# Kernel optimization log

Measured on AMD Instinct MI355X. Metric: run time of the kernel, lower is better.

## Reference

```python
import jax, jax.numpy as jnp
import numpy as np

DIM = 192
SHIFT = 3
PAD = SHIFT // 2  # 1
EPS = 1e-5


def conv1x1(x, w, b):
    # 1x1x1 Conv3d == channel matmul. x: (B,C,D,H,W), w: (O,C), b: (O,)
    return jnp.einsum('bcdhw,oc->bodhw', x, w) + b[None, :, None, None, None]


def group_norm1(x, w, b):
    # GroupNorm(1, C): normalize over (C,D,H,W) per sample, per-channel affine.
    mu = x.mean(axis=(1, 2, 3, 4), keepdims=True)
    var = x.var(axis=(1, 2, 3, 4), keepdims=True)
    xn = (x - mu) * jax.lax.rsqrt(var + EPS)
    return xn * w[None, :, None, None, None] + b[None, :, None, None, None]


def axial_shift(x, axis):
    # reflect-pad all 3 spatial dims, roll channel-chunks along `axis`, crop back.
    R = x.shape[-1]
    xp = jnp.pad(x, ((0, 0), (0, 0), (PAD, PAD), (PAD, PAD), (PAD, PAD)), mode='reflect')
    chunks = jnp.split(xp, SHIFT, axis=1)
    rolled = [jnp.roll(c, s, axis=axis) for c, s in zip(chunks, range(-PAD, PAD + 1))]
    xc = jnp.concatenate(rolled, axis=1)
    return xc[:, :, PAD:PAD + R, PAD:PAD + R, PAD:PAD + R]


def setup_inputs() -> dict:
    key = jax.random.key(0)
    ks = jax.random.split(key, 16)
    B, C, R = 8, DIM, 32
    x = jax.random.normal(ks[0], (B, C, R, R, R), dtype=jnp.float32)
    wmat = lambda k: jax.random.normal(k, (C, C), dtype=jnp.float32) * 0.05
    vec = lambda k: jax.random.normal(k, (C,), dtype=jnp.float32) * 0.05
    return {
        'x': x,
        'w1': wmat(ks[1]), 'b1': vec(ks[2]),
        'n1w': jnp.ones((C,), jnp.float32), 'n1b': jnp.zeros((C,), jnp.float32),
        'w21': wmat(ks[3]), 'b21': vec(ks[4]),
        'w22': wmat(ks[5]), 'b22': vec(ks[6]),
        'w23': wmat(ks[7]), 'b23': vec(ks[8]),
        'n2w': jnp.ones((C,), jnp.float32), 'n2b': jnp.zeros((C,), jnp.float32),
        'w3': wmat(ks[9]), 'b3': vec(ks[10]),
    }


def reference(x, w1, b1, n1w, n1b, w21, b21, w22, b22, w23, b23, n2w, n2b, w3, b3):
    h = conv1x1(x, w1, b1)
    h = group_norm1(h, n1w, n1b)
    h = jax.nn.gelu(h, approximate=False)
    h = axial_shift(h, axis=3)
    h = conv1x1(h, w22, b22)
    h = axial_shift(h, axis=2)
    h = conv1x1(h, w21, b21)
    h = axial_shift(h, axis=4)
    h = conv1x1(h, w23, b23)
    h = jax.nn.gelu(h, approximate=False)
    h = group_norm1(h, n2w, n2b)
    h = conv1x1(h, w3, b3)
    return h
```

## Files before the change

kernel.cpp:

```cpp
#include <hip/hip_runtime.h>
#include <math.h>

#define NCH 192
#define NB 8
#define SPAT 32768
#define TILES_PER_B 512
#define NBLK (NB * TILES_PER_B)
#define NELEM_PER_B ((size_t)NCH * SPAT)

typedef short s16x8 __attribute__((ext_vector_type(8)));
typedef float f32x4 __attribute__((ext_vector_type(4)));

__device__ __forceinline__ float bf2f(unsigned short h) {
  return __uint_as_float(((unsigned)h) << 16);
}
__device__ __forceinline__ unsigned short f2bf(float f) {
  unsigned u = __float_as_uint(f);
  u += 0x7FFF + ((u >> 16) & 1);
  return (unsigned short)(u >> 16);
}
__device__ __forceinline__ unsigned cvt_pk(float lo, float hi) {
  unsigned r;
  asm("v_cvt_pk_bf16_f32 %0, %1, %2" : "=v"(r) : "v"(lo), "v"(hi));
  return r;
}

__device__ __forceinline__ float gelu_f(float x) {
  float x2 = x * x;
  float z2 = x * fmaf(x2, 0.0713548163f, 1.5957769100f);
  float e = __expf(z2);
  float r = __builtin_amdgcn_rcpf(e + 1.0f);
  return fmaf(-r, x, x);
}

__device__ __forceinline__ int rshift(int i, int c) {
  int j = i - (c - 1);
  j = (j < 0) ? 1 : j;
  j = (j > 31) ? 30 : j;
  return j;
}

__device__ __forceinline__ int lds_off(int c, int p, int u) {
  return (c * 64 + p) * 128 + 16 * (((u >> 3) ^ (p & 7) ^ ((p >> 3) & 7)) & 7) + 2 * (u & 7);
}

template <int SHIFTW>
__device__ __forceinline__ void do_gemm48(const char* __restrict__ B,
                                          const unsigned short* __restrict__ wm,
                                          int wave, int col, int kg,
                                          f32x4 acc[3][4]) {
  const unsigned short* wp = wm + (wave * 48 + col) * NCH + kg * 8;
  s16x8 afc[3], afn[3];
#pragma unroll
  for (int r = 0; r < 3; ++r) afc[r] = *(const s16x8*)(wp + r * 16 * NCH);
#pragma unroll
  for (int ks = 0; ks < 6; ++ks) {
    if (ks < 5) {
#pragma unroll
      for (int r = 0; r < 3; ++r)
        afn[r] = *(const s16x8*)(wp + (ks + 1) * 32 + r * 16 * NCH);
    }
    int k0 = ks * 32 + kg * 8;
    int c = k0 >> 6, u = k0 & 63;
    s16x8 bf[4];
#pragma unroll
    for (int m = 0; m < 4; ++m) {
      int p = m * 16 + col;
      int ps = SHIFTW ? ((p & 32) | rshift(p & 31, c)) : p;
      bf[m] = *(const s16x8*)(B + lds_off(c, ps, u));
    }
#pragma unroll
    for (int r = 0; r < 3; ++r)
#pragma unroll
      for (int m = 0; m < 4; ++m)
        acc[r][m] = __builtin_amdgcn_mfma_f32_16x16x32_bf16(afc[r], bf[m], acc[r][m], 0, 0, 0);
#pragma unroll
    for (int r = 0; r < 3; ++r) afc[r] = afn[r];
  }
}

__device__ __forceinline__ void stats_reduce(float ssum, float ssq, int wave, int lane,
                                             float* red, float* partials, int blk) {
#pragma unroll
  for (int off = 1; off < 64; off <<= 1) {
    ssum += __shfl_xor(ssum, off, 64);
    ssq += __shfl_xor(ssq, off, 64);
  }
  if (lane == 0) { red[wave * 2] = ssum; red[wave * 2 + 1] = ssq; }
  __syncthreads();
  if (wave == 0 && lane == 0) {
    partials[blk * 2] = red[0] + red[2] + red[4] + red[6];
    partials[blk * 2 + 1] = red[1] + red[3] + red[5] + red[7];
  }
}

__device__ __forceinline__ void store_tile(const char* __restrict__ L, char* __restrict__ ob,
                                           int tid) {
  int G = tid & 7;
#pragma unroll
  for (int j = 0; j < 6; ++j) {
    const int c = j >> 1;
    int p = (j & 1) * 32 + (tid >> 3);
    s16x8 v = *(const s16x8*)(L + lds_off(c, p, G * 8));
    *(s16x8*)(ob + (size_t)p * 384 + (c * 8 + G) * 16) = v;
  }
}

__global__ __launch_bounds__(256, 4)
void pass1(const float* __restrict__ x, const unsigned short* __restrict__ w1b,
           const float* __restrict__ b1, unsigned short* __restrict__ out,
           float* __restrict__ partials) {
  __shared__ __align__(16) char B[3 * 64 * 128];
  __shared__ float red[8];
  int blk = blockIdx.x, b = blk >> 9, p0 = (blk & 511) * 64;
  int tid = threadIdx.x, wave = tid >> 6, lane = tid & 63;
  int col = lane & 15, kg = lane >> 4;

  const float* xb = x + (size_t)b * NELEM_PER_B + p0;
  int q = tid & 15;
#pragma unroll
  for (int j = 0; j < 6; ++j) {
    int chp = j * 16 + (tid >> 4);
    int ch0 = 2 * chp;
    int cc = chp >> 5, u0 = ch0 & 63;
    const float* s0 = xb + (size_t)ch0 * SPAT + 4 * q;
    f32x4 a = *(const f32x4*)s0;
    f32x4 c2 = *(const f32x4*)(s0 + SPAT);
#pragma unroll
    for (int i = 0; i < 4; ++i)
      *(unsigned*)(B + lds_off(cc, 4 * q + i, u0)) = cvt_pk(a[i], c2[i]);
  }
  __syncthreads();

  f32x4 acc[3][4] = {};
  do_gemm48<0>(B, w1b, wave, col, kg, acc);

  float ssum = 0.f, ssq = 0.f;
  __syncthreads();
#pragma unroll
  for (int r = 0; r < 3; ++r) {
    int rowb = wave * 48 + r * 16 + kg * 4;
    f32x4 bs = *(const f32x4*)(b1 + rowb);
#pragma unroll
    for (int m = 0; m < 4; ++m) {
      int p = m * 16 + col;
      float v0 = acc[r][m][0] + bs[0], v1 = acc[r][m][1] + bs[1];
      float v2 = acc[r][m][2] + bs[2], v3 = acc[r][m][3] + bs[3];
      ssum += (v0 + v1) + (v2 + v3);
      ssq = fmaf(v0, v0, fmaf(v1, v1, fmaf(v2, v2, fmaf(v3, v3, ssq))));
      uint2 pk; pk.x = cvt_pk(v0, v1); pk.y = cvt_pk(v2, v3);
      *(uint2*)(B + lds_off(rowb >> 6, p, rowb & 63)) = pk;
    }
  }
  __syncthreads();
  store_tile(B, (char*)out + ((size_t)b * SPAT + p0) * 384, tid);
  stats_reduce(ssum, ssq, wave, lane, red, partials, blk);
}

__global__ __launch_bounds__(256, 4)
void pass2a(const unsigned short* __restrict__ in, const unsigned short* __restrict__ w22b,
            const float* __restrict__ b22, unsigned short* __restrict__ out,
            const unsigned short* __restrict__ ACbf) {
  __shared__ __align__(16) char B[3 * 64 * 128];
  int blk = blockIdx.x, b = blk >> 9, p0 = (blk & 511) * 64;
  int tid = threadIdx.x, wave = tid >> 6, lane = tid & 63;
  int col = lane & 15, kg = lane >> 4;

  const char* ib = (const char*)in + (size_t)b * SPAT * 384;
  const unsigned short* acb = ACbf + b * 2 * NCH;
  int G = tid & 7;
#pragma unroll
  for (int j = 0; j < 6; ++j) {
    const int c = j >> 1;
    int p = (j & 1) * 32 + (tid >> 3);
    int h = ((p0 + p) >> 5) & 31;
    int sp = (p0 + p) + (rshift(h, c) - h) * 32;
    s16x8 v = *(const s16x8*)(ib + (size_t)sp * 384 + (c * 8 + G) * 16);
    s16x8 aA = *(const s16x8*)(acb + c * 64 + G * 8);
    s16x8 aC = *(const s16x8*)(acb + NCH + c * 64 + G * 8);
    unsigned w[4];
#pragma unroll
    for (int i = 0; i < 4; ++i) {
      float f0 = gelu_f(fmaf(bf2f((unsigned short)v[2 * i]), bf2f((unsigned short)aA[2 * i]),
                             bf2f((unsigned short)aC[2 * i])));
      float f1 = gelu_f(fmaf(bf2f((unsigned short)v[2 * i + 1]), bf2f((unsigned short)aA[2 * i + 1]),
                             bf2f((unsigned short)aC[2 * i + 1])));
      w[i] = cvt_pk(f0, f1);
    }
    *(uint2*)(B + lds_off(c, p, G * 8)) = make_uint2(w[0], w[1]);
    *(uint2*)(B + lds_off(c, p, G * 8 + 4)) = make_uint2(w[2], w[3]);
  }
  __syncthreads();

  f32x4 acc[3][4] = {};
  do_gemm48<0>(B, w22b, wave, col, kg, acc);
  __syncthreads();
#pragma unroll
  for (int r = 0; r < 3; ++r) {
    int rowb = wave * 48 + r * 16 + kg * 4;
    f32x4 bs = *(const f32x4*)(b22 + rowb);
#pragma unroll
    for (int m = 0; m < 4; ++m) {
      int p = m * 16 + col;
      uint2 pk;
      pk.x = cvt_pk(acc[r][m][0] + bs[0], acc[r][m][1] + bs[1]);
      pk.y = cvt_pk(acc[r][m][2] + bs[2], acc[r][m][3] + bs[3]);
      *(uint2*)(B + lds_off(rowb >> 6, p, rowb & 63)) = pk;
    }
  }
  __syncthreads();
  store_tile(B, (char*)out + ((size_t)b * SPAT + p0) * 384, tid);
}

__global__ __launch_bounds__(256, 4)
void pass2bc(const unsigned short* __restrict__ in, const unsigned short* __restrict__ w21b,
             const float* __restrict__ b21, const unsigned short* __restrict__ w23b,
             const float* __restrict__ b23, unsigned short* __restrict__ out,
             float* __restrict__ partials) {
  __shared__ __align__(16) char B[3 * 64 * 128];
  __shared__ float red[8];
  int blk = blockIdx.x, b = blk >> 9, p0 = (blk & 511) * 64;
  int tid = threadIdx.x, wave = tid >> 6, lane = tid & 63;
  int col = lane & 15, kg = lane >> 4;

  int d = p0 >> 10;
  int soff[3];
#pragma unroll
  for (int c = 0; c < 3; ++c) soff[c] = (rshift(d, c) - d) * 1024;

  const char* ib = (const char*)in + (size_t)b * SPAT * 384;
  int G = tid & 7;
#pragma unroll
  for (int j = 0; j < 6; ++j) {
    const int c = j >> 1;
    int p = (j & 1) * 32 + (tid >> 3);
    s16x8 v = *(const s16x8*)(ib + (size_t)(p0 + p + soff[c]) * 384 + (c * 8 + G) * 16);
    *(s16x8*)(B + lds_off(c, p, G * 8)) = v;
  }
  __syncthreads();

  f32x4 acc[3][4] = {};
  do_gemm48<0>(B, w21b, wave, col, kg, acc);
  __syncthreads();
#pragma unroll
  for (int r = 0; r < 3; ++r) {
    int rowb = wave * 48 + r * 16 + kg * 4;
    f32x4 bs = *(const f32x4*)(b21 + rowb);
#pragma unroll
    for (int m = 0; m < 4; ++m) {
      int p = m * 16 + col;
      uint2 pk;
      pk.x = cvt_pk(acc[r][m][0] + bs[0], acc[r][m][1] + bs[1]);
      pk.y = cvt_pk(acc[r][m][2] + bs[2], acc[r][m][3] + bs[3]);
      *(uint2*)(B + lds_off(rowb >> 6, p, rowb & 63)) = pk;
    }
  }
  __syncthreads();

#pragma unroll
  for (int r = 0; r < 3; ++r)
#pragma unroll
    for (int m = 0; m < 4; ++m) acc[r][m] = (f32x4){0.f, 0.f, 0.f, 0.f};
  do_gemm48<1>(B, w23b, wave, col, kg, acc);
  __syncthreads();

  float ssum = 0.f, ssq = 0.f;
#pragma unroll
  for (int r = 0; r < 3; ++r) {
    int rowb = wave * 48 + r * 16 + kg * 4;
    f32x4 bs = *(const f32x4*)(b23 + rowb);
#pragma unroll
    for (int m = 0; m < 4; ++m) {
      int p = m * 16 + col;
      float v0 = gelu_f(acc[r][m][0] + bs[0]), v1 = gelu_f(acc[r][m][1] + bs[1]);
      float v2 = gelu_f(acc[r][m][2] + bs[2]), v3 = gelu_f(acc[r][m][3] + bs[3]);
      ssum += (v0 + v1) + (v2 + v3);
      ssq = fmaf(v0, v0, fmaf(v1, v1, fmaf(v2, v2, fmaf(v3, v3, ssq))));
      uint2 pk; pk.x = cvt_pk(v0, v1); pk.y = cvt_pk(v2, v3);
      *(uint2*)(B + lds_off(rowb >> 6, p, rowb & 63)) = pk;
    }
  }
  __syncthreads();
  store_tile(B, (char*)out + ((size_t)b * SPAT + p0) * 384, tid);
  stats_reduce(ssum, ssq, wave, lane, red, partials, blk);
}

__global__ __launch_bounds__(256, 4)
void pass3(const unsigned short* __restrict__ in, const unsigned short* __restrict__ w3e,
           const float* __restrict__ b3e, float* __restrict__ outf) {
  __shared__ __align__(16) char B[3 * 64 * 128];
  int blk = blockIdx.x, b = blk >> 9, p0 = (blk & 511) * 64;
  int tid = threadIdx.x, wave = tid >> 6, lane = tid & 63;
  int col = lane & 15, kg = lane >> 4;

  const char* ib = (const char*)in + (size_t)b * SPAT * 384;
  int G = tid & 7;
#pragma unroll
  for (int j = 0; j < 6; ++j) {
    const int c = j >> 1;
    int p = (j & 1) * 32 + (tid >> 3);
    s16x8 v = *(const s16x8*)(ib + (size_t)(p0 + p) * 384 + (c * 8 + G) * 16);
    *(s16x8*)(B + lds_off(c, p, G * 8)) = v;
  }
  __syncthreads();

  f32x4 acc[3][4] = {};
  do_gemm48<0>(B, w3e + (size_t)b * NCH * NCH, wave, col, kg, acc);

  const float* bb = b3e + b * NCH;
#pragma unroll
  for (int r = 0; r < 3; ++r) {
    int rowb = wave * 48 + r * 16 + kg * 4;
    f32x4 bs = *(const f32x4*)(bb + rowb);
#pragma unroll
    for (int m = 0; m < 4; ++m) {
      int p = p0 + m * 16 + col;
#pragma unroll
      for (int j = 0; j < 4; ++j)
        outf[((size_t)b * NCH + rowb + j) * SPAT + p] = acc[r][m][j] + bs[j];
    }
  }
}

__global__ void stats_finalize(const float* __restrict__ partials,
                               const float* __restrict__ nw, const float* __restrict__ nb,
                               float* __restrict__ AC, unsigned short* __restrict__ ACbf) {
  int b = blockIdx.x, tid = threadIdx.x;
  __shared__ float s0[256], s1[256];
  float a = 0.f, c = 0.f;
  for (int i = tid; i < TILES_PER_B; i += 256) {
    a += partials[(b * TILES_PER_B + i) * 2];
    c += partials[(b * TILES_PER_B + i) * 2 + 1];
  }
  s0[tid] = a; s1[tid] = c;
  __syncthreads();
  for (int st = 128; st > 0; st >>= 1) {
    if (tid < st) { s0[tid] += s0[tid + st]; s1[tid] += s1[tid + st]; }
    __syncthreads();
  }
  float inv_n = 1.0f / (float)NELEM_PER_B;
  float mu = s0[0] * inv_n;
  float var = s1[0] * inv_n - mu * mu;
  float rs = rsqrtf(var + 1e-5f);
  if (tid < NCH) {
    float A = rs * nw[tid];
    float C = nb[tid] - mu * A;
    AC[b * 2 * NCH + tid] = A;
    AC[b * 2 * NCH + NCH + tid] = C;
    ACbf[b * 2 * NCH + tid] = f2bf(A);
    ACbf[b * 2 * NCH + NCH + tid] = f2bf(C);
  }
}

__global__ void prep_weights(const float* __restrict__ w1, const float* __restrict__ w21,
                             const float* __restrict__ w22, const float* __restrict__ w23,
                             unsigned short* __restrict__ wb) {
  int i = blockIdx.x * 256 + threadIdx.x;
  if (i >= 4 * NCH * NCH) return;
  int m = i / (NCH * NCH), r = i % (NCH * NCH);
  const float* src = (m == 0) ? w1 : (m == 1) ? w22 : (m == 2) ? w21 : w23;
  wb[i] = f2bf(src[r]);
}

__global__ void prep_w3(const float* __restrict__ w3, const float* __restrict__ b3,
                        const float* __restrict__ AC2,
                        unsigned short* __restrict__ w3e, float* __restrict__ b3e) {
  int b = blockIdx.x, o = threadIdx.x;
  if (o >= NCH) return;
  const float* A = AC2 + b * 2 * NCH;
  const float* C = A + NCH;
  float s = b3[o];
  for (int c = 0; c < NCH; ++c) {
    float w = w3[o * NCH + c];
    w3e[((size_t)b * NCH + o) * NCH + c] = f2bf(w * A[c]);
    s = fmaf(w, C[c], s);
  }
  b3e[b * NCH + o] = s;
}

extern "C" void kernel_launch(void* const* d_in, const int* in_sizes, int n_in,
                              void* d_out, int out_size, void* d_ws, size_t ws_size,
                              hipStream_t stream) {
  const float* x   = (const float*)d_in[0];
  const float* w1  = (const float*)d_in[1];
  const float* b1  = (const float*)d_in[2];
  const float* n1w = (const float*)d_in[3];
  const float* n1b = (const float*)d_in[4];
  const float* w21 = (const float*)d_in[5];
  const float* b21 = (const float*)d_in[6];
  const float* w22 = (const float*)d_in[7];
  const float* b22 = (const float*)d_in[8];
  const float* w23 = (const float*)d_in[9];
  const float* b23 = (const float*)d_in[10];
  const float* n2w = (const float*)d_in[11];
  const float* n2b = (const float*)d_in[12];
  const float* w3  = (const float*)d_in[13];
  const float* b3  = (const float*)d_in[14];

  char* ws = (char*)d_ws;
  size_t off = 0;
  unsigned short* wb = (unsigned short*)(ws + off); off += (size_t)4 * NCH * NCH * 2;
  off = (off + 255) & ~(size_t)255;
  unsigned short* w3e = (unsigned short*)(ws + off); off += (size_t)NB * NCH * NCH * 2;
  off = (off + 255) & ~(size_t)255;
  float* b3e = (float*)(ws + off); off += NB * NCH * 4;
  float* AC1 = (float*)(ws + off); off += NB * 2 * NCH * 4;
  float* AC2 = (float*)(ws + off); off += NB * 2 * NCH * 4;
  unsigned short* ACbf1 = (unsigned short*)(ws + off); off += NB * 2 * NCH * 2;
  unsigned short* ACbf2 = (unsigned short*)(ws + off); off += NB * 2 * NCH * 2;
  off = (off + 255) & ~(size_t)255;
  float* part1 = (float*)(ws + off); off += (size_t)NBLK * 2 * 4;
  float* part2 = (float*)(ws + off); off += (size_t)NBLK * 2 * 4;
  off = (off + 255) & ~(size_t)255;
  unsigned short* R1 = (unsigned short*)(ws + off);
  unsigned short* R2 = (unsigned short*)d_out;

  prep_weights<<<(4 * NCH * NCH + 255) / 256, 256, 0, stream>>>(w1, w21, w22, w23, wb);

  pass1<<<NBLK, 256, 0, stream>>>(x, wb + 0 * NCH * NCH, b1, R1, part1);
  stats_finalize<<<NB, 256, 0, stream>>>(part1, n1w, n1b, AC1, ACbf1);

  pass2a<<<NBLK, 256, 0, stream>>>(R1, wb + 1 * NCH * NCH, b22, R2, ACbf1);

  pass2bc<<<NBLK, 256, 0, stream>>>(R2, wb + 2 * NCH * NCH, b21,
                                    wb + 3 * NCH * NCH, b23, R1, part2);
  stats_finalize<<<NB, 256, 0, stream>>>(part2, n2w, n2b, AC2, ACbf2);
  prep_w3<<<NB, NCH, 0, stream>>>(w3, b3, AC2, w3e, b3e);

  pass3<<<NBLK, 256, 0, stream>>>(R1, w3e, b3e, (float*)d_out);
}
```

Before: 334.5 us.

## Double spatial tile to 128 positions with 512-thread blocks; parallelize prep_w3

Each block now covers 128 spatial positions with 8 waves instead of 64 positions with 4 waves. Four waves split the channels and two split the positions, so each weight fragment loaded from global memory is reused across twice as many positions. Staging loads and stores use a flat, fully coalesced indexing over the 384-byte position rows, and the per-tile shift is computed for every element. prep_w3 moves from 8 blocks with a serial 192-step loop to one 64-thread wavefront per output channel with a shuffle reduction. Per-block LDS doubles to 48 KB, which may cut the number of resident blocks per CU.

```diff
diff --git a/kernel.cpp b/kernel.cpp
--- a/kernel.cpp
+++ b/kernel.cpp
@@ -4,7 +4,8 @@
 #define NCH 192
 #define NB 8
 #define SPAT 32768
-#define TILES_PER_B 512
+#define POSB 128
+#define TILES_PER_B (SPAT / POSB)
 #define NBLK (NB * TILES_PER_B)
 #define NELEM_PER_B ((size_t)NCH * SPAT)
 
@@ -41,15 +42,15 @@
 }
 
 __device__ __forceinline__ int lds_off(int c, int p, int u) {
-  return (c * 64 + p) * 128 + 16 * (((u >> 3) ^ (p & 7) ^ ((p >> 3) & 7)) & 7) + 2 * (u & 7);
+  return (c * POSB + p) * 128 + 16 * (((u >> 3) ^ (p & 7) ^ ((p >> 3) & 7)) & 7) + 2 * (u & 7);
 }
 
 template <int SHIFTW>
 __device__ __forceinline__ void do_gemm48(const char* __restrict__ B,
                                           const unsigned short* __restrict__ wm,
-                                          int wave, int col, int kg,
+                                          int chb, int pbase, int col, int kg,
                                           f32x4 acc[3][4]) {
-  const unsigned short* wp = wm + (wave * 48 + col) * NCH + kg * 8;
+  const unsigned short* wp = wm + (chb * 48 + col) * NCH + kg * 8;
   s16x8 afc[3], afn[3];
 #pragma unroll
   for (int r = 0; r < 3; ++r) afc[r] = *(const s16x8*)(wp + r * 16 * NCH);
@@ -65,8 +66,8 @@
     s16x8 bf[4];
 #pragma unroll
     for (int m = 0; m < 4; ++m) {
-      int p = m * 16 + col;
-      int ps = SHIFTW ? ((p & 32) | rshift(p & 31, c)) : p;
+      int p = pbase + m * 16 + col;
+      int ps = SHIFTW ? ((p & ~31) | rshift(p & 31, c)) : p;
       bf[m] = *(const s16x8*)(B + lds_off(c, ps, u));
     }
 #pragma unroll
@@ -79,8 +80,65 @@
   }
 }
 
-__device__ __forceinline__ void stats_reduce(float ssum, float ssq, int wave, int lane,
-                                             float* red, float* partials, int blk) {
+template <int AX>
+__device__ __forceinline__ void stage_load8(const char* __restrict__ ib, int p0, int tid,
+                                            s16x8 vr[6]) {
+#pragma unroll
+  for (int j = 0; j < 6; ++j) {
+    int g = j * 512 + tid;
+    int p = g / 24, r24 = g - 24 * p;
+    int c = r24 >> 3;
+    int pp = p0 + p, sp = pp;
+    if (AX == 3) { int h = (pp >> 5) & 31; sp = pp + (rshift(h, c) - h) * 32; }
+    if (AX == 2) { int d = pp >> 10;       sp = pp + (rshift(d, c) - d) * 1024; }
+    vr[j] = *(const s16x8*)(ib + (size_t)sp * 384 + r24 * 16);
+  }
+}
+
+template <int FUSE>
+__device__ __forceinline__ void stage_write8(char* __restrict__ B, int tid, const s16x8 vr[6],
+                                             const unsigned short* __restrict__ acb) {
+#pragma unroll
+  for (int j = 0; j < 6; ++j) {
+    int g = j * 512 + tid;
+    int p = g / 24, r24 = g - 24 * p;
+    int c = r24 >> 3, gr = r24 & 7;
+    if (FUSE) {
+      int ch0 = r24 * 8;
+      s16x8 aA = *(const s16x8*)(acb + ch0);
+      s16x8 aC = *(const s16x8*)(acb + NCH + ch0);
+      unsigned w[4];
+#pragma unroll
+      for (int i = 0; i < 4; ++i) {
+        float f0 = gelu_f(fmaf(bf2f((unsigned short)vr[j][2 * i]),
+                               bf2f((unsigned short)aA[2 * i]),
+                               bf2f((unsigned short)aC[2 * i])));
+        float f1 = gelu_f(fmaf(bf2f((unsigned short)vr[j][2 * i + 1]),
+                               bf2f((unsigned short)aA[2 * i + 1]),
+                               bf2f((unsigned short)aC[2 * i + 1])));
+        w[i] = cvt_pk(f0, f1);
+      }
+      *(uint2*)(B + lds_off(c, p, gr * 8)) = make_uint2(w[0], w[1]);
+      *(uint2*)(B + lds_off(c, p, gr * 8 + 4)) = make_uint2(w[2], w[3]);
+    } else {
+      *(s16x8*)(B + lds_off(c, p, gr * 8)) = vr[j];
+    }
+  }
+}
+
+__device__ __forceinline__ void store_tile8(const char* __restrict__ L, char* __restrict__ ob,
+                                            int tid) {
+#pragma unroll
+  for (int j = 0; j < 6; ++j) {
+    int g = j * 512 + tid;
+    int p = g / 24, r24 = g - 24 * p;
+    s16x8 v = *(const s16x8*)(L + lds_off(r24 >> 3, p, (r24 & 7) * 8));
+    *(s16x8*)(ob + (size_t)g * 16) = v;
+  }
+}
+
+__device__ __forceinline__ void stats_reduce8(float ssum, float ssq, int wave, int lane,
+                                              float* red, float* partials, int blk) {
 #pragma unroll
   for (int off = 1; off < 64; off <<= 1) {
     ssum += __shfl_xor(ssum, off, 64);
@@ -89,38 +147,30 @@
   if (lane == 0) { red[wave * 2] = ssum; red[wave * 2 + 1] = ssq; }
   __syncthreads();
   if (wave == 0 && lane == 0) {
-    partials[blk * 2] = red[0] + red[2] + red[4] + red[6];
-    partials[blk * 2 + 1] = red[1] + red[3] + red[5] + red[7];
-  }
-}
-
-__device__ __forceinline__ void store_tile(const char* __restrict__ L, char* __restrict__ ob,
-                                           int tid) {
-  int G = tid & 7;
-#pragma unroll
-  for (int j = 0; j < 6; ++j) {
-    const int c = j >> 1;
-    int p = (j & 1) * 32 + (tid >> 3);
-    s16x8 v = *(const s16x8*)(L + lds_off(c, p, G * 8));
-    *(s16x8*)(ob + (size_t)p * 384 + (c * 8 + G) * 16) = v;
-  }
-}
-
-__global__ __launch_bounds__(256, 4)
+    float a = 0.f, c = 0.f;
+#pragma unroll
+    for (int w = 0; w < 8; ++w) { a += red[w * 2]; c += red[w * 2 + 1]; }
+    partials[blk * 2] = a;
+    partials[blk * 2 + 1] = c;
+  }
+}
+
+__global__ __launch_bounds__(512, 4)
 void pass1(const float* __restrict__ x, const unsigned short* __restrict__ w1b,
            const float* __restrict__ b1, unsigned short* __restrict__ out,
            float* __restrict__ partials) {
-  __shared__ __align__(16) char B[3 * 64 * 128];
-  __shared__ float red[8];
-  int blk = blockIdx.x, b = blk >> 9, p0 = (blk & 511) * 64;
+  __shared__ __align__(16) char B[3 * POSB * 128];
+  __shared__ float red[16];
+  int blk = blockIdx.x, b = blk >> 8, p0 = (blk & 255) * POSB;
   int tid = threadIdx.x, wave = tid >> 6, lane = tid & 63;
   int col = lane & 15, kg = lane >> 4;
+  int chb = wave & 3, pbase = (wave >> 2) * 64;
 
   const float* xb = x + (size_t)b * NELEM_PER_B + p0;
-  int q = tid & 15;
+  int q = tid & 31;
 #pragma unroll
   for (int j = 0; j < 6; ++j) {
-    int chp = j * 16 + (tid >> 4);
+    int chp = j * 16 + (tid >> 5);
     int ch0 = 2 * chp;
     int cc = chp >> 5, u0 = ch0 & 63;
     const float* s0 = xb + (size_t)ch0 * SPAT + 4 * q;
@@ -133,17 +183,17 @@
   __syncthreads();
 
   f32x4 acc[3][4] = {};
-  do_gemm48<0>(B, w1b, wave, col, kg, acc);
+  do_gemm48<0>(B, w1b, chb, pbase, col, kg, acc);
 
   float ssum = 0.f, ssq = 0.f;
   __syncthreads();
 #pragma unroll
   for (int r = 0; r < 3; ++r) {
-    int rowb = wave * 48 + r * 16 + kg * 4;
+    int rowb = chb * 48 + r * 16 + kg * 4;
     f32x4 bs = *(const f32x4*)(b1 + rowb);
 #pragma unroll
     for (int m = 0; m < 4; ++m) {
-      int p = m * 16 + col;
+      int p = pbase + m * 16 + col;
       float v0 = acc[r][m][0] + bs[0], v1 = acc[r][m][1] + bs[1];
       float v2 = acc[r][m][2] + bs[2], v3 = acc[r][m][3] + bs[3];
       ssum += (v0 + v1) + (v2 + v3);
@@ -153,55 +203,38 @@
     }
   }
   __syncthreads();
-  store_tile(B, (char*)out + ((size_t)b * SPAT + p0) * 384, tid);
-  stats_reduce(ssum, ssq, wave, lane, red, partials, blk);
-}
-
-__global__ __launch_bounds__(256, 4)
+  store_tile8(B, (char*)out + ((size_t)b * SPAT + p0) * 384, tid);
+  stats_reduce8(ssum, ssq, wave, lane, red, partials, blk);
+}
+
+__global__ __launch_bounds__(512, 4)
 void pass2a(const unsigned short* __restrict__ in, const unsigned short* __restrict__ w22b,
             const float* __restrict__ b22, unsigned short* __restrict__ out,
             const unsigned short* __restrict__ ACbf) {
-  __shared__ __align__(16) char B[3 * 64 * 128];
-  int blk = blockIdx.x, b = blk >> 9, p0 = (blk & 511) * 64;
+  __shared__ __align__(16) char B[3 * POSB * 128];
+  int blk = blockIdx.x, b = blk >> 8, p0 = (blk & 255) * POSB;
   int tid = threadIdx.x, wave = tid >> 6, lane = tid & 63;
   int col = lane & 15, kg = lane >> 4;
+  int chb = wave & 3, pbase = (wave >> 2) * 64;
 
   const char* ib = (const char*)in + (size_t)b * SPAT * 384;
   const unsigned short* acb = ACbf + b * 2 * NCH;
-  int G = tid & 7;
-#pragma unroll
-  for (int j = 0; j < 6; ++j) {
-    const int c = j >> 1;
-    int p = (j & 1) * 32 + (tid >> 3);
-    int h = ((p0 + p) >> 5) & 31;
-    int sp = (p0 + p) + (rshift(h, c) - h) * 32;
-    s16x8 v = *(const s16x8*)(ib + (size_t)sp * 384 + (c * 8 + G) * 16);
-    s16x8 aA = *(const s16x8*)(acb + c * 64 + G * 8);
-    s16x8 aC = *(const s16x8*)(acb + NCH + c * 64 + G * 8);
-    unsigned w[4];
-#pragma unroll
-    for (int i = 0; i < 4; ++i) {
-      float f0 = gelu_f(fmaf(bf2f((unsigned short)v[2 * i]), bf2f((unsigned short)aA[2 * i]),
-                             bf2f((unsigned short)aC[2 * i])));
-      float f1 = gelu_f(fmaf(bf2f((unsigned short)v[2 * i + 1]), bf2f((unsigned short)aA[2 * i + 1]),
-                             bf2f((unsigned short)aC[2 * i + 1])));
-      w[i] = cvt_pk(f0, f1);
-    }
-    *(uint2*)(B + lds_off(c, p, G * 8)) = make_uint2(w[0], w[1]);
-    *(uint2*)(B + lds_off(c, p, G * 8 + 4)) = make_uint2(w[2], w[3]);
-  }
+
+  s16x8 vr[6];
+  stage_load8<3>(ib, p0, tid, vr);
+  stage_write8<1>(B, tid, vr, acb);
   __syncthreads();
 
   f32x4 acc[3][4] = {};
-  do_gemm48<0>(B, w22b, wave, col, kg, acc);
+  do_gemm48<0>(B, w22b, chb, pbase, col, kg, acc);
   __syncthreads();
 #pragma unroll
   for (int r = 0; r < 3; ++r) {
-    int rowb = wave * 48 + r * 16 + kg * 4;
+    int rowb = chb * 48 + r * 16 + kg * 4;
     f32x4 bs = *(const f32x4*)(b22 + rowb);
 #pragma unroll
     for (int m = 0; m < 4; ++m) {
-      int p = m * 16 + col;
+      int p = pbase + m * 16 + col;
       uint2 pk;
       pk.x = cvt_pk(acc[r][m][0] + bs[0], acc[r][m][1] + bs[1]);
       pk.y = cvt_pk(acc[r][m][2] + bs[2], acc[r][m][3] + bs[3]);
@@ -209,46 +242,38 @@
     }
   }
   __syncthreads();
-  store_tile(B, (char*)out + ((size_t)b * SPAT + p0) * 384, tid);
-}
-
-__global__ __launch_bounds__(256, 4)
+  store_tile8(B, (char*)out + ((size_t)b * SPAT + p0) * 384, tid);
+}
+
+__global__ __launch_bounds__(512, 4)
 void pass2bc(const unsigned short* __restrict__ in, const unsigned short* __restrict__ w21b,
              const float* __restrict__ b21, const unsigned short* __restrict__ w23b,
              const float* __restrict__ b23, unsigned short* __restrict__ out,
              float* __restrict__ partials) {
-  __shared__ __align__(16) char B[3 * 64 * 128];
-  __shared__ float red[8];
-  int blk = blockIdx.x, b = blk >> 9, p0 = (blk & 511) * 64;
+  __shared__ __align__(16) char B[3 * POSB * 128];
+  __shared__ float red[16];
+  int blk = blockIdx.x, b = blk >> 8, p0 = (blk & 255) * POSB;
   int tid = threadIdx.x, wave = tid >> 6, lane = tid & 63;
   int col = lane & 15, kg = lane >> 4;
-
-  int d = p0 >> 10;
-  int soff[3];
-#pragma unroll
-  for (int c = 0; c < 3; ++c) soff[c] = (rshift(d, c) - d) * 1024;
+  int chb = wave & 3, pbase = (wave >> 2) * 64;
 
   const char* ib = (const char*)in + (size_t)b * SPAT * 384;
-  int G = tid & 7;
-#pragma unroll
-  for (int j = 0; j < 6; ++j) {
-    const int c = j >> 1;
-    int p = (j & 1) * 32 + (tid >> 3);
-    s16x8 v = *(const s16x8*)(ib + (size_t)(p0 + p + soff[c]) * 384 + (c * 8 + G) * 16);
-    *(s16x8*)(B + lds_off(c, p, G * 8)) = v;
-  }
+
+  s16x8 vr[6];
+  stage_load8<2>(ib, p0, tid, vr);
+  stage_write8<0>(B, tid, vr, nullptr);
   __syncthreads();
 
   f32x4 acc[3][4] = {};
-  do_gemm48<0>(B, w21b, wave, col, kg, acc);
+  do_gemm48<0>(B, w21b, chb, pbase, col, kg, acc);
   __syncthreads();
 #pragma unroll
   for (int r = 0; r < 3; ++r) {
-    int rowb = wave * 48 + r * 16 + kg * 4;
+    int rowb = chb * 48 + r * 16 + kg * 4;
     f32x4 bs = *(const f32x4*)(b21 + rowb);
 #pragma unroll
     for (int m = 0; m < 4; ++m) {
-      int p = m * 16 + col;
+      int p = pbase + m * 16 + col;
       uint2 pk;
       pk.x = cvt_pk(acc[r][m][0] + bs[0], acc[r][m][1] + bs[1]);
       pk.y = cvt_pk(acc[r][m][2] + bs[2], acc[r][m][3] + bs[3]);
@@ -261,17 +286,17 @@
   for (int r = 0; r < 3; ++r)
 #pragma unroll
     for (int m = 0; m < 4; ++m) acc[r][m] = (f32x4){0.f, 0.f, 0.f, 0.f};
-  do_gemm48<1>(B, w23b, wave, col, kg, acc);
+  do_gemm48<1>(B, w23b, chb, pbase, col, kg, acc);
   __syncthreads();
 
   float ssum = 0.f, ssq = 0.f;
 #pragma unroll
   for (int r = 0; r < 3; ++r) {
-    int rowb = wave * 48 + r * 16 + kg * 4;
+    int rowb = chb * 48 + r * 16 + kg * 4;
     f32x4 bs = *(const f32x4*)(b23 + rowb);
 #pragma unroll
     for (int m = 0; m < 4; ++m) {
-      int p = m * 16 + col;
+      int p = pbase + m * 16 + col;
       float v0 = gelu_f(acc[r][m][0] + bs[0]), v1 = gelu_f(acc[r][m][1] + bs[1]);
       float v2 = gelu_f(acc[r][m][2] + bs[2]), v3 = gelu_f(acc[r][m][3] + bs[3]);
       ssum += (v0 + v1) + (v2 + v3);
@@ -281,40 +306,37 @@
     }
   }
   __syncthreads();
-  store_tile(B, (char*)out + ((size_t)b * SPAT + p0) * 384, tid);
-  stats_reduce(ssum, ssq, wave, lane, red, partials, blk);
-}
-
-__global__ __launch_bounds__(256, 4)
+  store_tile8(B, (char*)out + ((size_t)b * SPAT + p0) * 384, tid);
+  stats_reduce8(ssum, ssq, wave, lane, red, partials, blk);
+}
+
+__global__ __launch_bounds__(512, 4)
 void pass3(const unsigned short* __restrict__ in, const unsigned short* __restrict__ w3e,
            const float* __restrict__ b3e, float* __restrict__ outf) {
-  __shared__ __align__(16) char B[3 * 64 * 128];
-  int blk = blockIdx.x, b = blk >> 9, p0 = (blk & 511) * 64;
+  __shared__ __align__(16) char B[3 * POSB * 128];
+  int blk = blockIdx.x, b = blk >> 8, p0 = (blk & 255) * POSB;
   int tid = threadIdx.x, wave = tid >> 6, lane = tid & 63;
   int col = lane & 15, kg = lane >> 4;
+  int chb = wave & 3, pbase = (wave >> 2) * 64;
 
   const char* ib = (const char*)in + (size_t)b * SPAT * 384;
-  int G = tid & 7;
-#pragma unroll
-  for (int j = 0; j < 6; ++j) {
-    const int c = j >> 1;
-    int p = (j & 1) * 32 + (tid >> 3);
-    s16x8 v = *(const s16x8*)(ib + (size_t)(p0 + p) * 384 + (c * 8 + G) * 16);
-    *(s16x8*)(B + lds_off(c, p, G * 8)) = v;
-  }
+
+  s16x8 vr[6];
+  stage_load8<0>(ib, p0, tid, vr);
+  stage_write8<0>(B, tid, vr, nullptr);
   __syncthreads();
 
   f32x4 acc[3][4] = {};
-  do_gemm48<0>(B, w3e + (size_t)b * NCH * NCH, wave, col, kg, acc);
+  do_gemm48<0>(B, w3e + (size_t)b * NCH * NCH, chb, pbase, col, kg, acc);
 
   const float* bb = b3e + b * NCH;
 #pragma unroll
   for (int r = 0; r < 3; ++r) {
-    int rowb = wave * 48 + r * 16 + kg * 4;
+    int rowb = chb * 48 + r * 16 + kg * 4;
     f32x4 bs = *(const f32x4*)(bb + rowb);
 #pragma unroll
     for (int m = 0; m < 4; ++m) {
-      int p = p0 + m * 16 + col;
+      int p = p0 + pbase + m * 16 + col;
 #pragma unroll
       for (int j = 0; j < 4; ++j)
         outf[((size_t)b * NCH + rowb + j) * SPAT + p] = acc[r][m][j] + bs[j];
@@ -324,13 +346,14 @@
 
 __global__ void stats_finalize(const float* __restrict__ partials,
                                const float* __restrict__ nw, const float* __restrict__ nb,
-                               float* __restrict__ AC, unsigned short* __restrict__ ACbf) {
+                               float* __restrict__ AC, unsigned short* __restrict__ ACbf,
+                               int nper) {
   int b = blockIdx.x, tid = threadIdx.x;
   __shared__ float s0[256], s1[256];
   float a = 0.f, c = 0.f;
-  for (int i = tid; i < TILES_PER_B; i += 256) {
-    a += partials[(b * TILES_PER_B + i) * 2];
-    c += partials[(b * TILES_PER_B + i) * 2 + 1];
+  for (int i = tid; i < nper; i += 256) {
+    a += partials[(b * nper + i) * 2];
+    c += partials[(b * nper + i) * 2 + 1];
   }
   s0[tid] = a; s1[tid] = c;
   __syncthreads();
@@ -362,20 +385,25 @@
   wb[i] = f2bf(src[r]);
 }
 
-__global__ void prep_w3(const float* __restrict__ w3, const float* __restrict__ b3,
-                        const float* __restrict__ AC2,
-                        unsigned short* __restrict__ w3e, float* __restrict__ b3e) {
-  int b = blockIdx.x, o = threadIdx.x;
-  if (o >= NCH) return;
+__global__ void prep_w3p(const float* __restrict__ w3, const float* __restrict__ b3,
+                         const float* __restrict__ AC2,
+                         unsigned short* __restrict__ w3e, float* __restrict__ b3e) {
+  int gb = blockIdx.x;
+  int b = gb / NCH, o = gb - b * NCH;
   const float* A = AC2 + b * 2 * NCH;
   const float* C = A + NCH;
-  float s = b3[o];
-  for (int c = 0; c < NCH; ++c) {
+  int lane = threadIdx.x;
+  float s = 0.f;
+#pragma unroll
+  for (int k = 0; k < 3; ++k) {
+    int c = k * 64 + lane;
     float w = w3[o * NCH + c];
     w3e[((size_t)b * NCH + o) * NCH + c] = f2bf(w * A[c]);
     s = fmaf(w, C[c], s);
   }
-  b3e[b * NCH + o] = s;
+#pragma unroll
+  for (int off = 1; off < 64; off <<= 1) s += __shfl_xor(s, off, 64);
+  if (lane == 0) b3e[b * NCH + o] = b3[o] + s;
 }
 
 extern "C" void kernel_launch(void* const* d_in, const int* in_sizes, int n_in,
@@ -417,15 +445,15 @@
 
   prep_weights<<<(4 * NCH * NCH + 255) / 256, 256, 0, stream>>>(w1, w21, w22, w23, wb);
 
-  pass1<<<NBLK, 256, 0, stream>>>(x, wb + 0 * NCH * NCH, b1, R1, part1);
-  stats_finalize<<<NB, 256, 0, stream>>>(part1, n1w, n1b, AC1, ACbf1);
-
-  pass2a<<<NBLK, 256, 0, stream>>>(R1, wb + 1 * NCH * NCH, b22, R2, ACbf1);
-
-  pass2bc<<<NBLK, 256, 0, stream>>>(R2, wb + 2 * NCH * NCH, b21,
+  pass1<<<NBLK, 512, 0, stream>>>(x, wb + 0 * NCH * NCH, b1, R1, part1);
+  stats_finalize<<<NB, 256, 0, stream>>>(part1, n1w, n1b, AC1, ACbf1, TILES_PER_B);
+
+  pass2a<<<NBLK, 512, 0, stream>>>(R1, wb + 1 * NCH * NCH, b22, R2, ACbf1);
+
+  pass2bc<<<NBLK, 512, 0, stream>>>(R2, wb + 2 * NCH * NCH, b21,
                                     wb + 3 * NCH * NCH, b23, R1, part2);
-  stats_finalize<<<NB, 256, 0, stream>>>(part2, n2w, n2b, AC2, ACbf2);
-  prep_w3<<<NB, NCH, 0, stream>>>(w3, b3, AC2, w3e, b3e);
-
-  pass3<<<NBLK, 256, 0, stream>>>(R1, w3e, b3e, (float*)d_out);
-}
+  stats_finalize<<<NB, 256, 0, stream>>>(part2, n2w, n2b, AC2, ACbf2, TILES_PER_B);
+  prep_w3p<<<NB * NCH, 64, 0, stream>>>(w3, b3, AC2, w3e, b3e);
+
+  pass3<<<NBLK, 512, 0, stream>>>(R1, w3e, b3e, (float*)d_out);
+}
```

After: 344.8 us. 3.1% more time.

## Fold GroupNorm stats finalize into consumer kernels and apply norm2 on load

Applied to the files above, without the earlier changes.

Removes the separate stats_finalize and prep_w3 launches. Each block of pass2a and pass3 now reduces the 512 per-tile partials for its batch, computes the per-channel scale and shift in shared memory, and applies them while loading its tile. Norm2 is no longer folded into per-batch w3 weights. It is applied element-wise before the GEMM against a shared bf16 w3. This saves three small serialized launches, at the cost of every block redundantly reading 4 KB of partials and doing an extra reduction and sync.

```diff
diff --git a/kernel.cpp b/kernel.cpp
--- a/kernel.cpp
+++ b/kernel.cpp
@@ -92,6 +92,34 @@
     partials[blk * 2] = red[0] + red[2] + red[4] + red[6];
     partials[blk * 2 + 1] = red[1] + red[3] + red[5] + red[7];
   }
+}
+
+__device__ __forceinline__ void stats_inline(const float* __restrict__ partials, int b,
+                                             const float* __restrict__ nw,
+                                             const float* __restrict__ nb,
+                                             float* __restrict__ acs, float* __restrict__ red,
+                                             int tid, int wave, int lane) {
+  f32x4 v = *(const f32x4*)(partials + ((size_t)b * TILES_PER_B + 2 * tid) * 2);
+  float a = v[0] + v[2], c = v[1] + v[3];
+#pragma unroll
+  for (int off = 1; off < 64; off <<= 1) {
+    a += __shfl_xor(a, off, 64);
+    c += __shfl_xor(c, off, 64);
+  }
+  if (lane == 0) { red[wave * 2] = a; red[wave * 2 + 1] = c; }
+  __syncthreads();
+  float sum = red[0] + red[2] + red[4] + red[6];
+  float sq = red[1] + red[3] + red[5] + red[7];
+  float inv_n = 1.0f / (float)NELEM_PER_B;
+  float mu = sum * inv_n;
+  float var = sq * inv_n - mu * mu;
+  float rs = rsqrtf(var + 1e-5f);
+  if (tid < NCH) {
+    float A = rs * nw[tid];
+    acs[tid] = A;
+    acs[NCH + tid] = nb[tid] - mu * A;
+  }
+  __syncthreads();
 }
 
 __device__ __forceinline__ void store_tile(const char* __restrict__ L, char* __restrict__ ob,
@@ -160,14 +188,18 @@
 __global__ __launch_bounds__(256, 4)
 void pass2a(const unsigned short* __restrict__ in, const unsigned short* __restrict__ w22b,
             const float* __restrict__ b22, unsigned short* __restrict__ out,
-            const unsigned short* __restrict__ ACbf) {
+            const float* __restrict__ part1,
+            const float* __restrict__ n1w, const float* __restrict__ n1b) {
   __shared__ __align__(16) char B[3 * 64 * 128];
+  __shared__ __align__(16) float acs[2 * NCH];
+  __shared__ float red[8];
   int blk = blockIdx.x, b = blk >> 9, p0 = (blk & 511) * 64;
   int tid = threadIdx.x, wave = tid >> 6, lane = tid & 63;
   int col = lane & 15, kg = lane >> 4;
 
+  stats_inline(part1, b, n1w, n1b, acs, red, tid, wave, lane);
+
   const char* ib = (const char*)in + (size_t)b * SPAT * 384;
-  const unsigned short* acb = ACbf + b * 2 * NCH;
   int G = tid & 7;
 #pragma unroll
   for (int j = 0; j < 6; ++j) {
@@ -176,15 +208,18 @@
     int h = ((p0 + p) >> 5) & 31;
     int sp = (p0 + p) + (rshift(h, c) - h) * 32;
     s16x8 v = *(const s16x8*)(ib + (size_t)sp * 384 + (c * 8 + G) * 16);
-    s16x8 aA = *(const s16x8*)(acb + c * 64 + G * 8);
-    s16x8 aC = *(const s16x8*)(acb + NCH + c * 64 + G * 8);
+    int ch0 = c * 64 + G * 8;
+    f32x4 a0 = *(const f32x4*)(acs + ch0), a1 = *(const f32x4*)(acs + ch0 + 4);
+    f32x4 c0 = *(const f32x4*)(acs + NCH + ch0), c1 = *(const f32x4*)(acs + NCH + ch0 + 4);
     unsigned w[4];
 #pragma unroll
     for (int i = 0; i < 4; ++i) {
-      float f0 = gelu_f(fmaf(bf2f((unsigned short)v[2 * i]), bf2f((unsigned short)aA[2 * i]),
-                             bf2f((unsigned short)aC[2 * i])));
-      float f1 = gelu_f(fmaf(bf2f((unsigned short)v[2 * i + 1]), bf2f((unsigned short)aA[2 * i + 1]),
-                             bf2f((unsigned short)aC[2 * i + 1])));
+      float A0 = (i < 2) ? a0[2 * i] : a1[2 * i - 4];
+      float A1 = (i < 2) ? a0[2 * i + 1] : a1[2 * i - 3];
+      float C0 = (i < 2) ? c0[2 * i] : c1[2 * i - 4];
+      float C1 = (i < 2) ? c0[2 * i + 1] : c1[2 * i - 3];
+      float f0 = gelu_f(fmaf(bf2f((unsigned short)v[2 * i]), A0, C0));
+      float f1 = gelu_f(fmaf(bf2f((unsigned short)v[2 * i + 1]), A1, C1));
       w[i] = cvt_pk(f0, f1);
     }
     *(uint2*)(B + lds_off(c, p, G * 8)) = make_uint2(w[0], w[1]);
@@ -286,12 +321,18 @@
 }
 
 __global__ __launch_bounds__(256, 4)
-void pass3(const unsigned short* __restrict__ in, const unsigned short* __restrict__ w3e,
-           const float* __restrict__ b3e, float* __restrict__ outf) {
+void pass3(const unsigned short* __restrict__ in, const unsigned short* __restrict__ w3b,
+           const float* __restrict__ b3, float* __restrict__ outf,
+           const float* __restrict__ part2,
+           const float* __restrict__ n2w, const float* __restrict__ n2b) {
   __shared__ __align__(16) char B[3 * 64 * 128];
+  __shared__ __align__(16) float acs[2 * NCH];
+  __shared__ float red[8];
   int blk = blockIdx.x, b = blk >> 9, p0 = (blk & 511) * 64;
   int tid = threadIdx.x, wave = tid >> 6, lane = tid & 63;
   int col = lane & 15, kg = lane >> 4;
+
+  stats_inline(part2, b, n2w, n2b, acs, red, tid, wave, lane);
 
   const char* ib = (const char*)in + (size_t)b * SPAT * 384;
   int G = tid & 7;
@@ -300,18 +341,32 @@
     const int c = j >> 1;
     int p = (j & 1) * 32 + (tid >> 3);
     s16x8 v = *(const s16x8*)(ib + (size_t)(p0 + p) * 384 + (c * 8 + G) * 16);
-    *(s16x8*)(B + lds_off(c, p, G * 8)) = v;
+    int ch0 = c * 64 + G * 8;
+    f32x4 a0 = *(const f32x4*)(acs + ch0), a1 = *(const f32x4*)(acs + ch0 + 4);
+    f32x4 c0 = *(const f32x4*)(acs + NCH + ch0), c1 = *(const f32x4*)(acs + NCH + ch0 + 4);
+    unsigned w[4];
+#pragma unroll
+    for (int i = 0; i < 4; ++i) {
+      float A0 = (i < 2) ? a0[2 * i] : a1[2 * i - 4];
+      float A1 = (i < 2) ? a0[2 * i + 1] : a1[2 * i - 3];
+      float C0 = (i < 2) ? c0[2 * i] : c1[2 * i - 4];
+      float C1 = (i < 2) ? c0[2 * i + 1] : c1[2 * i - 3];
+      float f0 = fmaf(bf2f((unsigned short)v[2 * i]), A0, C0);
+      float f1 = fmaf(bf2f((unsigned short)v[2 * i + 1]), A1, C1);
+      w[i] = cvt_pk(f0, f1);
+    }
+    *(uint2*)(B + lds_off(c, p, G * 8)) = make_uint2(w[0], w[1]);
+    *(uint2*)(B + lds_off(c, p, G * 8 + 4)) = make_uint2(w[2], w[3]);
   }
   __syncthreads();
 
   f32x4 acc[3][4] = {};
-  do_gemm48<0>(B, w3e + (size_t)b * NCH * NCH, wave, col, kg, acc);
-
-  const float* bb = b3e + b * NCH;
+  do_gemm48<0>(B, w3b, wave, col, kg, acc);
+
 #pragma unroll
   for (int r = 0; r < 3; ++r) {
     int rowb = wave * 48 + r * 16 + kg * 4;
-    f32x4 bs = *(const f32x4*)(bb + rowb);
+    f32x4 bs = *(const f32x4*)(b3 + rowb);
 #pragma unroll
     for (int m = 0; m < 4; ++m) {
       int p = p0 + m * 16 + col;
@@ -322,60 +377,15 @@
   }
 }
 
-__global__ void stats_finalize(const float* __restrict__ partials,
-                               const float* __restrict__ nw, const float* __restrict__ nb,
-                               float* __restrict__ AC, unsigned short* __restrict__ ACbf) {
-  int b = blockIdx.x, tid = threadIdx.x;
-  __shared__ float s0[256], s1[256];
-  float a = 0.f, c = 0.f;
-  for (int i = tid; i < TILES_PER_B; i += 256) {
-    a += partials[(b * TILES_PER_B + i) * 2];
-    c += partials[(b * TILES_PER_B + i) * 2 + 1];
-  }
-  s0[tid] = a; s1[tid] = c;
-  __syncthreads();
-  for (int st = 128; st > 0; st >>= 1) {
-    if (tid < st) { s0[tid] += s0[tid + st]; s1[tid] += s1[tid + st]; }
-    __syncthreads();
-  }
-  float inv_n = 1.0f / (float)NELEM_PER_B;
-  float mu = s0[0] * inv_n;
-  float var = s1[0] * inv_n - mu * mu;
-  float rs = rsqrtf(var + 1e-5f);
-  if (tid < NCH) {
-    float A = rs * nw[tid];
-    float C = nb[tid] - mu * A;
-    AC[b * 2 * NCH + tid] = A;
-    AC[b * 2 * NCH + NCH + tid] = C;
-    ACbf[b * 2 * NCH + tid] = f2bf(A);
-    ACbf[b * 2 * NCH + NCH + tid] = f2bf(C);
-  }
-}
-
 __global__ void prep_weights(const float* __restrict__ w1, const float* __restrict__ w21,
                              const float* __restrict__ w22, const float* __restrict__ w23,
+                             const float* __restrict__ w3,
                              unsigned short* __restrict__ wb) {
   int i = blockIdx.x * 256 + threadIdx.x;
-  if (i >= 4 * NCH * NCH) return;
+  if (i >= 5 * NCH * NCH) return;
   int m = i / (NCH * NCH), r = i % (NCH * NCH);
-  const float* src = (m == 0) ? w1 : (m == 1) ? w22 : (m == 2) ? w21 : w23;
+  const float* src = (m == 0) ? w1 : (m == 1) ? w22 : (m == 2) ? w21 : (m == 3) ? w23 : w3;
   wb[i] = f2bf(src[r]);
-}
-
-__global__ void prep_w3(const float* __restrict__ w3, const float* __restrict__ b3,
-                        const float* __restrict__ AC2,
-                        unsigned short* __restrict__ w3e, float* __restrict__ b3e) {
-  int b = blockIdx.x, o = threadIdx.x;
-  if (o >= NCH) return;
-  const float* A = AC2 + b * 2 * NCH;
-  const float* C = A + NCH;
-  float s = b3[o];
-  for (int c = 0; c < NCH; ++c) {
-    float w = w3[o * NCH + c];
-    w3e[((size_t)b * NCH + o) * NCH + c] = f2bf(w * A[c]);
-    s = fmaf(w, C[c], s);
-  }
-  b3e[b * NCH + o] = s;
 }
 
 extern "C" void kernel_launch(void* const* d_in, const int* in_sizes, int n_in,
@@ -399,15 +409,7 @@
 
   char* ws = (char*)d_ws;
   size_t off = 0;
-  unsigned short* wb = (unsigned short*)(ws + off); off += (size_t)4 * NCH * NCH * 2;
-  off = (off + 255) & ~(size_t)255;
-  unsigned short* w3e = (unsigned short*)(ws + off); off += (size_t)NB * NCH * NCH * 2;
-  off = (off + 255) & ~(size_t)255;
-  float* b3e = (float*)(ws + off); off += NB * NCH * 4;
-  float* AC1 = (float*)(ws + off); off += NB * 2 * NCH * 4;
-  float* AC2 = (float*)(ws + off); off += NB * 2 * NCH * 4;
-  unsigned short* ACbf1 = (unsigned short*)(ws + off); off += NB * 2 * NCH * 2;
-  unsigned short* ACbf2 = (unsigned short*)(ws + off); off += NB * 2 * NCH * 2;
+  unsigned short* wb = (unsigned short*)(ws + off); off += (size_t)5 * NCH * NCH * 2;
   off = (off + 255) & ~(size_t)255;
   float* part1 = (float*)(ws + off); off += (size_t)NBLK * 2 * 4;
   float* part2 = (float*)(ws + off); off += (size_t)NBLK * 2 * 4;
@@ -415,17 +417,15 @@
   unsigned short* R1 = (unsigned short*)(ws + off);
   unsigned short* R2 = (unsigned short*)d_out;
 
-  prep_weights<<<(4 * NCH * NCH + 255) / 256, 256, 0, stream>>>(w1, w21, w22, w23, wb);
+  prep_weights<<<(5 * NCH * NCH + 255) / 256, 256, 0, stream>>>(w1, w21, w22, w23, w3, wb);
 
   pass1<<<NBLK, 256, 0, stream>>>(x, wb + 0 * NCH * NCH, b1, R1, part1);
-  stats_finalize<<<NB, 256, 0, stream>>>(part1, n1w, n1b, AC1, ACbf1);
-
-  pass2a<<<NBLK, 256, 0, stream>>>(R1, wb + 1 * NCH * NCH, b22, R2, ACbf1);
+
+  pass2a<<<NBLK, 256, 0, stream>>>(R1, wb + 1 * NCH * NCH, b22, R2, part1, n1w, n1b);
 
   pass2bc<<<NBLK, 256, 0, stream>>>(R2, wb + 2 * NCH * NCH, b21,
                                     wb + 3 * NCH * NCH, b23, R1, part2);
-  stats_finalize<<<NB, 256, 0, stream>>>(part2, n2w, n2b, AC2, ACbf2);
-  prep_w3<<<NB, NCH, 0, stream>>>(w3, b3, AC2, w3e, b3e);
-
-  pass3<<<NBLK, 256, 0, stream>>>(R1, w3e, b3e, (float*)d_out);
-}
+
+  pass3<<<NBLK, 256, 0, stream>>>(R1, wb + 4 * NCH * NCH, b3, (float*)d_out,
+                                  part2, n2w, n2b);
+}
```

Measured after the change: 313.3 us. 1.07x faster.
